# Kernel tuning notes

Measured on AMD Instinct MI355X. Metric: run time of the kernel, lower is better.

The kernel has to match this reference:

```python
import jax, jax.numpy as jnp
import numpy as np

HID = 128
MAX_NODES = 100000
MAX_EDGES = 300000
EVT_LEN = 4096
NUM_NODE = 20000
NUM_EDGE = 320000
# EVENT_TYPE_ID_MAP: pad=0 start=1 end=2 node-add=3 node-delete=4 edge-add=5 edge-delete=6
NODE_ADD, NODE_DEL = 3, 4


def time_encode(t, time_w, time_b):
    # TimeEncoder: cos(Linear(1 -> hidden)(t))
    return jnp.cos(t[..., None] * time_w + time_b)


def gru_cell(x, h, w_ih, w_hh, b_ih, b_hh):
    gi = x @ w_ih.T + b_ih
    gh = h @ w_hh.T + b_hh
    i_r, i_z, i_n = jnp.split(gi, 3, axis=-1)
    h_r, h_z, h_n = jnp.split(gh, 3, axis=-1)
    r = jax.nn.sigmoid(i_r + h_r)
    z = jax.nn.sigmoid(i_z + h_z)
    n = jnp.tanh(i_n + r * h_n)
    return (1.0 - z) * n + z * h


def setup_inputs() -> dict:
    key = jax.random.key(0)
    ks = jax.random.split(key, 32)
    H = HID
    s = 0.05
    inp = {}
    inp["event_type_ids"] = jax.random.randint(ks[0], (EVT_LEN,), 0, 7)
    inp["src_ids"] = jax.random.randint(ks[1], (EVT_LEN,), 0, MAX_NODES)
    inp["src_mask"] = (jax.random.uniform(ks[2], (EVT_LEN,)) > 0.3).astype(jnp.float32)
    inp["dst_ids"] = jax.random.randint(ks[3], (EVT_LEN,), 0, MAX_NODES)
    inp["dst_mask"] = (jax.random.uniform(ks[4], (EVT_LEN,)) > 0.3).astype(jnp.float32)
    inp["event_edge_ids"] = jax.random.randint(ks[5], (EVT_LEN,), 0, MAX_EDGES)
    inp["event_embeddings"] = jax.random.normal(ks[6], (EVT_LEN, H), dtype=jnp.float32)
    inp["event_mask"] = (jax.random.uniform(ks[7], (EVT_LEN,)) > 0.2).astype(jnp.float32)
    inp["event_timestamps"] = jax.random.uniform(ks[8], (EVT_LEN,)) * 100.0
    inp["node_ids"] = jax.random.randint(ks[9], (NUM_NODE,), 0, MAX_NODES)
    inp["edge_ids"] = jax.random.randint(ks[10], (NUM_EDGE,), 0, MAX_EDGES)
    inp["edge_index"] = jax.random.randint(ks[11], (2, NUM_EDGE), 0, NUM_NODE)
    inp["time"] = 100
    # persistent-buffer state
    inp["memory"] = jax.random.normal(ks[12], (MAX_NODES, H), dtype=jnp.float32) * s
    inp["last_update"] = jax.random.uniform(ks[13], (MAX_EDGES,)) * 50.0
    inp["node_features"] = jax.random.normal(ks[14], (MAX_NODES, H), dtype=jnp.float32) * s
    inp["edge_features"] = jax.random.normal(ks[15], (MAX_EDGES, H), dtype=jnp.float32) * s
    # TimeEncoder params (Linear(1, H))
    inp["time_w"] = jax.random.normal(ks[16], (H,), dtype=jnp.float32) * s
    inp["time_b"] = jax.random.normal(ks[17], (H,), dtype=jnp.float32) * s
    # GRUCell(5H -> H)
    inp["gru_w_ih"] = jax.random.normal(ks[18], (3 * H, 5 * H), dtype=jnp.float32) * s
    inp["gru_w_hh"] = jax.random.normal(ks[19], (3 * H, H), dtype=jnp.float32) * s
    inp["gru_b_ih"] = jax.random.normal(ks[20], (3 * H,), dtype=jnp.float32) * s
    inp["gru_b_hh"] = jax.random.normal(ks[21], (3 * H,), dtype=jnp.float32) * s
    # TransformerConv(H, H, heads=1, edge_dim=2H)
    inp["wq"] = jax.random.normal(ks[22], (H, H), dtype=jnp.float32) * s
    inp["bq"] = jax.random.normal(ks[23], (H,), dtype=jnp.float32) * s
    inp["wk"] = jax.random.normal(ks[24], (H, H), dtype=jnp.float32) * s
    inp["bk"] = jax.random.normal(ks[25], (H,), dtype=jnp.float32) * s
    inp["wv"] = jax.random.normal(ks[26], (H, H), dtype=jnp.float32) * s
    inp["bv"] = jax.random.normal(ks[27], (H,), dtype=jnp.float32) * s
    inp["we"] = jax.random.normal(ks[28], (H, 2 * H), dtype=jnp.float32) * s  # lin_edge, no bias
    inp["wskip"] = jax.random.normal(ks[29], (H, H), dtype=jnp.float32) * s
    inp["bskip"] = jax.random.normal(ks[30], (H,), dtype=jnp.float32) * s
    return inp


def reference(event_type_ids, src_ids, src_mask, dst_ids, dst_mask, event_edge_ids,
              event_embeddings, event_mask, event_timestamps, node_ids, edge_ids,
              edge_index, time, memory, last_update, node_features, edge_features,
              time_w, time_b, gru_w_ih, gru_w_hh, gru_b_ih, gru_b_hh,
              wq, bq, wk, bk, wv, bv, we, wskip, bskip):
    H = HID
    # ---- message() ----
    L = event_type_ids.shape[0]
    type_embs = jnp.broadcast_to(event_type_ids[:, None].astype(memory.dtype), (L, H))
    src_embs = memory[src_ids] * src_mask[:, None]
    dst_embs = memory[dst_ids] * dst_mask[:, None]
    edge_last = last_update[event_edge_ids]
    rel_ts = event_timestamps - edge_last * dst_mask
    is_node_ev = ((event_type_ids == NODE_ADD) | (event_type_ids == NODE_DEL)).astype(event_timestamps.dtype)
    ts_emb = time_encode(event_timestamps * is_node_ev + rel_ts * dst_mask, time_w, time_b) * event_mask[:, None]
    src_msgs = jnp.concatenate([type_embs, src_embs, dst_embs, ts_emb, event_embeddings], axis=1) * event_mask[:, None]
    dst_msgs = jnp.concatenate([type_embs, dst_embs, src_embs, ts_emb, event_embeddings], axis=1) * dst_mask[:, None]
    # ---- agg_message(): scatter-mean over node ids ----
    def agg(msgs, ids):
        s = jax.ops.segment_sum(msgs, ids, num_segments=MAX_NODES)
        c = jax.ops.segment_sum(jnp.ones((msgs.shape[0],), msgs.dtype), ids, num_segments=MAX_NODES)
        return s / jnp.maximum(c, 1.0)[:, None]
    agg_src = agg(src_msgs, src_ids)
    agg_dst = agg(dst_msgs, dst_ids)
    # ---- GRU memory update on unique ids ----
    # torch: memory[cat(uniq_src, uniq_dst)] = rnn(...); reads use pre-update memory,
    # dst writes come after src writes so they override on overlap. Duplicate ids in
    # src_ids carry identical per-id values, so scatter-set is equivalent to unique().
    new_src = gru_cell(agg_src[src_ids], memory[src_ids], gru_w_ih, gru_w_hh, gru_b_ih, gru_b_hh)
    new_dst = gru_cell(agg_dst[dst_ids], memory[dst_ids], gru_w_ih, gru_w_hh, gru_b_ih, gru_b_hh)
    memory = memory.at[src_ids].set(new_src)
    memory = memory.at[dst_ids].set(new_dst)
    # ---- edge attributes ----
    rel_t = time - last_update[edge_ids]
    rel_t_embs = time_encode(rel_t, time_w, time_b)
    edge_attr = jnp.concatenate([rel_t_embs, edge_features[edge_ids]], axis=-1)  # (E, 2H)
    # ---- TransformerConv (heads=1, concat, root_weight) ----
    x = node_features[node_ids] + memory[node_ids]  # (N, H)
    src, dst = edge_index[0], edge_index[1]
    q = x @ wq.T + bq
    k = x @ wk.T + bk
    v = x @ wv.T + bv
    e = edge_attr @ we.T  # lin_edge (no bias)
    alpha = jnp.sum(q[dst] * (k[src] + e), axis=-1) / jnp.sqrt(jnp.asarray(H, x.dtype))
    amax = jax.ops.segment_max(alpha, dst, num_segments=x.shape[0])
    ex = jnp.exp(alpha - amax[dst])
    denom = jax.ops.segment_sum(ex, dst, num_segments=x.shape[0])
    p = ex / jnp.maximum(denom[dst], 1e-16)
    out = jax.ops.segment_sum(p[:, None] * (v[src] + e), dst, num_segments=x.shape[0])
    return out + x @ wskip.T + bskip
```

## Files before the change

kernel.cpp:

```cpp
#include <hip/hip_runtime.h>
#include <math.h>

#define HID   128
#define MAXN  100000
#define MAXE  300000
#define EVT   4096
#define NNODE 20000
#define NEDGE 320000

typedef unsigned short u16;
typedef __attribute__((ext_vector_type(8))) short bf16x8;
typedef __attribute__((ext_vector_type(4))) float f32x4;

#define OFF_WIHB      0u
#define OFF_WHHB      491520u
#define OFF_WEB       589824u
#define OFF_WALLB     655360u
#define OFF_BALL      851968u
#define BASE2         855040u
#define OFF_HEAD_SRC  (BASE2 + 0u)
#define OFF_HEAD_DST  (BASE2 + 400128u)
#define OFF_CNT_SRC   (BASE2 + 800256u)
#define OFF_CNT_DST   (BASE2 + 1200384u)
#define OFF_CHAIN_SRC (BASE2 + 1600512u)
#define OFF_CHAIN_DST (BASE2 + 1616896u)
#define OFF_XGB       (BASE2 + 22572032u)
#define OFF_HG        (BASE2 + 33057792u)
#define OFF_HGB       (BASE2 + 37252096u)
#define OFF_GI        (BASE2 + 39349248u)
#define OFF_GH        (BASE2 + 51932160u)
#define OFF_XB        (BASE2 + 1703936u)
#define OFF_QKVSE     (BASE2 + 7000064u)
#undef OFF_XB
#undef OFF_QKVSE
#define OFF_XB        (BASE2 + 1703936u)
#define OFF_QKVSE     (BASE2 + 6823936u)
#define OFF_KVB       (BASE2 + 68263936u)
#define OFF_DEG       (BASE2 + 78503936u)
#define OFF_OFFS      (BASE2 + 78584064u)
#define OFF_CURSOR    (BASE2 + 78664192u)
#define OFF_SORTED    (BASE2 + 78744320u)
#define OFF_SACCB     (BASE2 + 80024320u)

__device__ __forceinline__ float sigmoidf_(float x) { return 1.f / (1.f + __expf(-x)); }
__device__ __forceinline__ u16 f2b(float f) {
    unsigned u = __float_as_uint(f);
    unsigned r = (u + 0x7fffu + ((u >> 16) & 1u)) >> 16;
    return (u16)r;
}
__device__ __forceinline__ float b2f(unsigned h) { return __uint_as_float(h << 16); }

__global__ void k_prep(const float* __restrict__ w_ih, const float* __restrict__ w_hh,
                       const float* __restrict__ we,
                       const float* __restrict__ wq, const float* __restrict__ wk_,
                       const float* __restrict__ wv, const float* __restrict__ wskip,
                       const float* __restrict__ bq, const float* __restrict__ bk,
                       const float* __restrict__ bv, const float* __restrict__ bskip,
                       u16* __restrict__ w_ih_b, u16* __restrict__ w_hh_b,
                       u16* __restrict__ we_b, u16* __restrict__ Wallb,
                       float* __restrict__ ball, int* __restrict__ deg,
                       char* __restrict__ zbase) {
    int b = blockIdx.x, t = threadIdx.x;
    if (b < 960) {
        int i = b * 256 + t;
        w_ih_b[i] = f2b(w_ih[i]);
        return;
    }
    b -= 960;
    if (b < 192) {
        int i = b * 256 + t;
        w_hh_b[i] = f2b(w_hh[i]);
        return;
    }
    b -= 192;
    if (b < 128) {
        int i = b * 256 + t;
        we_b[i] = f2b(we[i]);
        return;
    }
    b -= 128;
    if (b < 79) {
        int i = b * 256 + t;
        if (i < NNODE) deg[i] = 0;
        return;
    }
    b -= 79;
    if (b < 384) {
        int idx = b * 256 + t;
        int row = idx >> 7;
        int k = idx & 127;
        float v;
        if (row < 128)      v = wq[row * 128 + k];
        else if (row < 256) v = wk_[(row - 128) * 128 + k];
        else if (row < 384) v = wv[(row - 256) * 128 + k];
        else if (row < 512) v = wskip[(row - 384) * 128 + k];
        else {
            int j = row - 512;
            float a = 0.f;
            for (int t2 = 0; t2 < 128; t2++) a += wq[t2 * 128 + k] * we[t2 * 256 + j];
            v = a;
        }
        Wallb[row * 128 + k] = f2b(v);
        if (k == 0) {
            float bb;
            if (row < 128)      bb = bq[row];
            else if (row < 256) bb = bk[row - 128];
            else if (row < 384) bb = bv[row - 256];
            else if (row < 512) bb = bskip[row - 384];
            else { int j = row - 512; float a = 0.f; for (int t2 = 0; t2 < 128; t2++) a += bq[t2] * we[t2 * 256 + j]; bb = a; }
            ball[row] = bb;
        }
        return;
    }
    b -= 384;
    const int NFF = 50016;
    uint4 ff = make_uint4(0xFFFFFFFFu, 0xFFFFFFFFu, 0xFFFFFFFFu, 0xFFFFFFFFu);
    uint4 zz = make_uint4(0u, 0u, 0u, 0u);
    int idx = b * 256 + t;
    int stride = 257 * 256;
    uint4* pff = (uint4*)zbase;
    uint4* pzz = (uint4*)(zbase + 800256);
    for (int i = idx; i < NFF; i += stride) pff[i] = ff;
    for (int i = idx; i < NFF; i += stride) pzz[i] = zz;
}

__global__ void k_msg_tables(const int* __restrict__ et_ids, const int* __restrict__ src_ids,
                          const float* __restrict__ src_mask, const int* __restrict__ dst_ids,
                          const float* __restrict__ dst_mask, const int* __restrict__ ev_eids,
                          const float* __restrict__ ev_emb, const float* __restrict__ ev_mask,
                          const float* __restrict__ ev_ts, const float* __restrict__ memory,
                          const float* __restrict__ last_update, const float* __restrict__ time_w,
                          const float* __restrict__ time_b,
                          int* __restrict__ head_src, int* __restrict__ head_dst,
                          int* __restrict__ cnt_src, int* __restrict__ cnt_dst,
                          int* __restrict__ chain_src, int* __restrict__ chain_dst,
                          const int* __restrict__ eidx, int* __restrict__ deg,
                          u16* __restrict__ Xgb, float* __restrict__ Hg, u16* __restrict__ Hgb) {
    int b = blockIdx.x, t = threadIdx.x;
    if (b >= EVT) {
        int bb = b - EVT;
        if (bb < 32) {
            int i = bb * 128 + t;
            int s = src_ids[i], d = dst_ids[i];
            chain_src[i] = atomicExch(&head_src[s], i);
            atomicAdd(&cnt_src[s], 1);
            chain_dst[i] = atomicExch(&head_dst[d], i);
            atomicAdd(&cnt_dst[d], 1);
        } else {
            int j = (bb - 32) * 128 + t;
            atomicAdd(&deg[eidx[NEDGE + j]], 1);
        }
        return;
    }
    int i = b;
    int c = t;
    int et = et_ids[i];
    float sm = src_mask[i], dm = dst_mask[i], em = ev_mask[i], ts = ev_ts[i];
    int sid = src_ids[i], did = dst_ids[i], eid = ev_eids[i];
    float isnode = (et == 3 || et == 4) ? 1.f : 0.f;
    float rel = ts - last_update[eid] * dm;
    float tval = ts * isnode + rel * dm;
    float tse = __cosf(tval * time_w[c] + time_b[c]) * em;
    float typ = (float)et;
    float sv_raw = memory[(size_t)sid * HID + c];
    float dv_raw = memory[(size_t)did * HID + c];
    float sv = sv_raw * sm;
    float dv = dv_raw * dm;
    float ev = ev_emb[(size_t)i * HID + c];
    Hg[(size_t)i * HID + c] = sv_raw;
    Hgb[(size_t)i * HID + c] = f2b(sv_raw);
    Hg[(size_t)(EVT + i) * HID + c] = dv_raw;
    Hgb[(size_t)(EVT + i) * HID + c] = f2b(dv_raw);
    u16* xs = Xgb + (size_t)i * 640;
    xs[c] = f2b(typ * em); xs[128 + c] = f2b(sv * em); xs[256 + c] = f2b(dv * em);
    xs[384 + c] = f2b(tse * em); xs[512 + c] = f2b(ev * em);
    u16* xd = Xgb + (size_t)(EVT + i) * 640;
    xd[c] = f2b(typ * dm); xd[128 + c] = f2b(dv * dm); xd[256 + c] = f2b(sv * dm);
    xd[384 + c] = f2b(tse * dm); xd[512 + c] = f2b(ev * dm);
}

__global__ void k_fix(const int* __restrict__ src_ids, const int* __restrict__ dst_ids,
                      const int* __restrict__ head_src, const int* __restrict__ head_dst,
                      const int* __restrict__ chain_src, const int* __restrict__ chain_dst,
                      const int* __restrict__ cnt_src, const int* __restrict__ cnt_dst,
                      const int* __restrict__ et_ids, const float* __restrict__ src_mask,
                      const float* __restrict__ dst_mask, const int* __restrict__ ev_eids,
                      const float* __restrict__ ev_emb, const float* __restrict__ ev_mask,
                      const float* __restrict__ ev_ts, const float* __restrict__ memory,
                      const float* __restrict__ last_update, const float* __restrict__ time_w,
                      const float* __restrict__ time_b, u16* __restrict__ Xgb) {
    int r = blockIdx.x, c = threadIdx.x;
    bool is_src = (r < EVT);
    int id = is_src ? src_ids[r] : dst_ids[r - EVT];
    int cnt = is_src ? cnt_src[id] : cnt_dst[id];
    if (cnt < 2) return;
    float own = memory[(size_t)id * HID + c];
    float tw = time_w[c], tb = time_b[c];
    float a0 = 0.f, a1 = 0.f, a2 = 0.f, a3 = 0.f, a4 = 0.f;
    int j = is_src ? head_src[id] : head_dst[id];
    for (int k = 0; k < cnt; ++k) {
        int et = et_ids[j];
        float sm = src_mask[j], dm = dst_mask[j], em = ev_mask[j], ts = ev_ts[j];
        int eid = ev_eids[j];
        float isnode = (et == 3 || et == 4) ? 1.f : 0.f;
        float rel = ts - last_update[eid] * dm;
        float tval = ts * isnode + rel * dm;
        float tse = __cosf(tval * tw + tb);
        float ev = ev_emb[(size_t)j * HID + c];
        float typ = (float)et;
        if (is_src) {
            float sv = own * sm;
            float dv = memory[(size_t)dst_ids[j] * HID + c] * dm;
            float tsm = tse * em;
            a0 += typ * em; a1 += sv * em; a2 += dv * em;
            a3 += tsm * em; a4 += ev * em;
            j = chain_src[j];
        } else {
            float dv = own * dm;
            float sv = memory[(size_t)src_ids[j] * HID + c] * sm;
            float tsm = tse * em;
            a0 += typ * dm; a1 += dv * dm; a2 += sv * dm;
            a3 += tsm * dm; a4 += ev * dm;
            j = chain_dst[j];
        }
    }
    float inv = 1.f / (float)cnt;
    u16* x = Xgb + (size_t)r * 640;
    x[c] = f2b(a0 * inv); x[128 + c] = f2b(a1 * inv); x[256 + c] = f2b(a2 * inv);
    x[384 + c] = f2b(a3 * inv); x[512 + c] = f2b(a4 * inv);
}

__device__ __forceinline__ void gemm_tile(const u16* __restrict__ A, const u16* __restrict__ W,
                                          const float* __restrict__ bias, float* __restrict__ C,
                                          u16* __restrict__ KVb, int M, int N, int K, int acc,
                                          u16* Als, u16* Wls) {
    int tid = threadIdx.x;
    int bm = blockIdx.x * 128, bn = blockIdx.y * 128;
    int wave = tid >> 6, lane = tid & 63;
    int wm = (wave & 1) * 64, wn = (wave >> 1) * 64;
    int l15 = lane & 15, quad = lane >> 4;
    f32x4 accf[4][4] = {};
    for (int k0 = 0; k0 < K; k0 += 32) {
#pragma unroll
        for (int h = 0; h < 2; ++h) {
            int ch = tid + h * 256;
            int row = ch >> 2, kc = (ch & 3) * 8;
            int gr = bm + row;
            float4 av = make_float4(0.f, 0.f, 0.f, 0.f);
            if (gr < M) av = *(const float4*)(A + (size_t)gr * K + k0 + kc);
            *(float4*)&Als[row * 40 + kc] = av;
            int wr = bn + row;
            float4 wv_ = *(const float4*)(W + (size_t)wr * K + k0 + kc);
            *(float4*)&Wls[row * 40 + kc] = wv_;
        }
        __syncthreads();
        bf16x8 af[4], bfr[4];
#pragma unroll
        for (int r = 0; r < 4; ++r)
            af[r] = *(const bf16x8*)&Als[(wm + r * 16 + l15) * 40 + quad * 8];
#pragma unroll
        for (int c2 = 0; c2 < 4; ++c2)
            bfr[c2] = *(const bf16x8*)&Wls[(wn + c2 * 16 + l15) * 40 + quad * 8];
#pragma unroll
        for (int r = 0; r < 4; ++r)
#pragma unroll
            for (int c2 = 0; c2 < 4; ++c2)
                accf[r][c2] = __builtin_amdgcn_mfma_f32_16x16x32_bf16(af[r], bfr[c2], accf[r][c2], 0, 0, 0);
        __syncthreads();
    }
#pragma unroll
    for (int r = 0; r < 4; ++r) {
#pragma unroll
        for (int c2 = 0; c2 < 4; ++c2) {
            int ncol = bn + wn + c2 * 16 + l15;
            float bv = bias ? bias[ncol] : 0.f;
#pragma unroll
            for (int reg = 0; reg < 4; ++reg) {
                int mrow = bm + wm + r * 16 + quad * 4 + reg;
                if (mrow >= M) continue;
                float v = accf[r][c2][reg] + bv;
                if (KVb && ncol >= 128 && ncol < 384) {
                    KVb[(size_t)mrow * 256 + (ncol - 128)] = f2b(v);
                } else {
                    if (acc) v += C[(size_t)mrow * N + ncol];
                    C[(size_t)mrow * N + ncol] = v;
                }
            }
        }
    }
}

__global__ __launch_bounds__(256) void k_gemm_mfma(const u16* __restrict__ A,
                                                   const u16* __restrict__ W,
                                                   const float* __restrict__ bias,
                                                   float* __restrict__ C,
                                                   u16* __restrict__ KVb,
                                                   int M, int N, int K, int acc) {
    __shared__ u16 Als[128 * 40];
    __shared__ u16 Wls[128 * 40];
    gemm_tile(A, W, bias, C, KVb, M, N, K, acc, Als, Wls);
}

__global__ __launch_bounds__(256) void k_gemm_qkvse(const u16* __restrict__ A,
                                                    const u16* __restrict__ W,
                                                    const float* __restrict__ bias,
                                                    float* __restrict__ C,
                                                    u16* __restrict__ KVb,
                                                    const int* __restrict__ eidx,
                                                    int* __restrict__ cursor,
                                                    int* __restrict__ sorted) {
    __shared__ u16 Als[128 * 40];
    __shared__ u16 Wls[128 * 40];
    if (blockIdx.y == 6) {
        int j = blockIdx.x * 256 + threadIdx.x;
        for (; j < NEDGE; j += 157 * 256) {
            int d = eidx[NEDGE + j];
            int pos = atomicAdd(&cursor[d], 1);
            sorted[pos] = j;
        }
        return;
    }
    gemm_tile(A, W, bias, C, KVb, NNODE, 768, 128, 0, Als, Wls);
}

__global__ __launch_bounds__(256) void k_gemm_dual(const u16* __restrict__ A0, const u16* __restrict__ W0,
                                                   const float* __restrict__ b0, float* __restrict__ C0,
                                                   const u16* __restrict__ A1, const u16* __restrict__ W1,
                                                   const float* __restrict__ b1, float* __restrict__ C1) {
    __shared__ u16 Als[128 * 40];
    __shared__ u16 Wls[128 * 40];
    if (blockIdx.z == 0) gemm_tile(A0, W0, b0, C0, nullptr, 2 * EVT, 384, 640, 0, Als, Wls);
    else                 gemm_tile(A1, W1, b1, C1, nullptr, 2 * EVT, 384, 128, 0, Als, Wls);
}

__global__ void k_gru_scatter(const float* __restrict__ Gi, const float* __restrict__ Gh,
                              const float* __restrict__ Hg, const int* __restrict__ src_ids,
                              const int* __restrict__ dst_ids, const int* __restrict__ cnt_dst,
                              float* __restrict__ memory) {
    int r = blockIdx.x, c = threadIdx.x;
    const float* gi = Gi + (size_t)r * 384;
    const float* gh = Gh + (size_t)r * 384;
    float rg = sigmoidf_(gi[c] + gh[c]);
    float z  = sigmoidf_(gi[128 + c] + gh[128 + c]);
    float n  = tanhf(gi[256 + c] + rg * gh[256 + c]);
    float h0 = Hg[(size_t)r * HID + c];
    float h  = (1.f - z) * n + z * h0;
    if (r < EVT) {
        int sid = src_ids[r];
        if (cnt_dst[sid] == 0) memory[(size_t)sid * HID + c] = h;
    } else {
        int did = dst_ids[r - EVT];
        memory[(size_t)did * HID + c] = h;
    }
}

__global__ __launch_bounds__(1024) void k_x_scan(const int* __restrict__ node_ids,
                                                 const float* __restrict__ nf,
                                                 const float* __restrict__ memory,
                                                 u16* __restrict__ Xb,
                                                 const int* __restrict__ deg,
                                                 int* __restrict__ offs,
                                                 int* __restrict__ cursor) {
    __shared__ int wsum[16];
    int p = blockIdx.x, t = threadIdx.x;
    if (p < 2500) {
        int row = p * 8 + (t >> 7), c = t & 127;
        int nid = node_ids[row];
        Xb[(size_t)row * HID + c] = f2b(nf[(size_t)nid * HID + c] + memory[(size_t)nid * HID + c]);
        return;
    }
    int lane = t & 63, w = t >> 6;
    int carry = 0;
    const int N4 = NNODE / 4;
    for (int base = 0; base < N4; base += 1024) {
        int i4 = base + t;
        int4 v = make_int4(0, 0, 0, 0);
        if (i4 < N4) v = ((const int4*)deg)[i4];
        int s = v.x + v.y + v.z + v.w;
        int x = s;
#pragma unroll
        for (int d = 1; d < 64; d <<= 1) { int y = __shfl_up(x, d, 64); if (lane >= d) x += y; }
        if (lane == 63) wsum[w] = x;
        __syncthreads();
        int add = 0, tot = 0;
        for (int k2 = 0; k2 < 16; ++k2) { int ss = wsum[k2]; if (k2 < w) add += ss; tot += ss; }
        if (i4 < N4) {
            int e = carry + add + x - s;
            int4 o;
            o.x = e;
            o.y = e + v.x;
            o.z = o.y + v.y;
            o.w = o.z + v.z;
            ((int4*)offs)[i4] = o;
            ((int4*)cursor)[i4] = o;
        }
        carry += tot;
        __syncthreads();
    }
    if (t == 0) offs[NNODE] = NEDGE;
}

__global__ __launch_bounds__(256) void k_node(const float* __restrict__ QK,
        const u16* __restrict__ KVb, const int* __restrict__ offs,
        const int* __restrict__ sorted, const int* __restrict__ eidx,
        const int* __restrict__ edge_ids, const float* __restrict__ last_update,
        const float* __restrict__ time_w, const float* __restrict__ time_b,
        const float* __restrict__ ef, const int* __restrict__ tptr,
        float* __restrict__ out, u16* __restrict__ saccb) {
    int wave = threadIdx.x >> 6, lane = threadIdx.x & 63;
    int n = blockIdx.x * 4 + wave;
    int c = 2 * lane;
    const float* base = QK + (size_t)n * 768;
    float2 qd   = *(const float2*)(base + c);
    float2 skip = *(const float2*)(base + 384 + c);
    float2 qet  = *(const float2*)(base + 512 + c);
    float2 qef  = *(const float2*)(base + 640 + c);
    float2 tw   = *(const float2*)(time_w + c);
    float2 tb   = *(const float2*)(time_b + c);
    float tf = (float)(*tptr);
    int start = offs[n], end = offs[n + 1];
    int deg = end - start;
    if (deg == 0) {
        *(float2*)(out + (size_t)n * HID + c) = skip;
        *(unsigned*)(saccb + (size_t)n * 256 + c) = 0u;
        *(unsigned*)(saccb + (size_t)n * 256 + 128 + c) = 0u;
        return;
    }
    float m = -1e30f, l_ = 0.f;
    float va0 = 0.f, va1 = 0.f, s00 = 0.f, s01 = 0.f, s10 = 0.f, s11 = 0.f;
    for (int cb = start; cb < end; cb += 64) {
        int cnt = end - cb; if (cnt > 64) cnt = 64;
        int s_l = 0, eid_l = 0; float rt_l = 0.f;
        if (lane < cnt) {
            int j = sorted[cb + lane];
            s_l = eidx[j];
            eid_l = edge_ids[j];
            rt_l = tf - last_update[eid_l];
        }
        for (int e0 = 0; e0 < cnt; e0 += 4) {
            float pv[4], cv0[4], cv1[4], vx[4], vy[4], ex[4], ey[4];
#pragma unroll
            for (int i = 0; i < 4; ++i) {
                int idx = e0 + i;
                int sel = (idx < cnt) ? idx : e0;
                int s   = __shfl(s_l, sel, 64);
                int eid = __shfl(eid_l, sel, 64);
                float rt = __shfl(rt_l, sel, 64);
                unsigned kvp = *(const unsigned*)(KVb + (size_t)s * 256 + c);
                unsigned vvp = *(const unsigned*)(KVb + (size_t)s * 256 + 128 + c);
                float2 ev = *(const float2*)(ef + (size_t)eid * HID + c);
                float k0f = b2f(kvp & 0xffffu), k1f = b2f(kvp >> 16);
                vx[i] = b2f(vvp & 0xffffu); vy[i] = b2f(vvp >> 16);
                cv0[i] = __cosf(rt * tw.x + tb.x);
                cv1[i] = __cosf(rt * tw.y + tb.y);
                ex[i] = ev.x; ey[i] = ev.y;
                pv[i] = qd.x * k0f + qd.y * k1f + qet.x * cv0[i] + qet.y * cv1[i]
                      + qef.x * ev.x + qef.y * ev.y;
            }
#pragma unroll
            for (int msk = 32; msk > 0; msk >>= 1) {
#pragma unroll
                for (int i = 0; i < 4; ++i) pv[i] += __shfl_xor(pv[i], msk, 64);
            }
            float al[4];
#pragma unroll
            for (int i = 0; i < 4; ++i)
                al[i] = (e0 + i < cnt) ? pv[i] * 0.08838834764831845f : -1e30f;
            float gm = fmaxf(fmaxf(al[0], al[1]), fmaxf(al[2], al[3]));
            if (gm > m) {
                float fac = __expf(m - gm);
                l_ *= fac; va0 *= fac; va1 *= fac;
                s00 *= fac; s01 *= fac; s10 *= fac; s11 *= fac;
                m = gm;
            }
#pragma unroll
            for (int i = 0; i < 4; ++i) {
                float w = __expf(al[i] - m);
                l_ += w;
                va0 += w * vx[i]; va1 += w * vy[i];
                s00 += w * cv0[i]; s01 += w * cv1[i];
                s10 += w * ex[i]; s11 += w * ey[i];
            }
        }
    }
    float inv = 1.f / fmaxf(l_, 1e-16f);
    float2 o; o.x = va0 * inv + skip.x; o.y = va1 * inv + skip.y;
    *(float2*)(out + (size_t)n * HID + c) = o;
    unsigned p0 = (unsigned)f2b(s00 * inv) | ((unsigned)f2b(s01 * inv) << 16);
    unsigned p1 = (unsigned)f2b(s10 * inv) | ((unsigned)f2b(s11 * inv) << 16);
    *(unsigned*)(saccb + (size_t)n * 256 + c) = p0;
    *(unsigned*)(saccb + (size_t)n * 256 + 128 + c) = p1;
}

extern "C" void kernel_launch(void* const* d_in, const int* in_sizes, int n_in,
                              void* d_out, int out_size, void* d_ws, size_t ws_size,
                              hipStream_t stream) {
    const int*   et_ids        = (const int*)d_in[0];
    const int*   src_ids       = (const int*)d_in[1];
    const float* src_mask      = (const float*)d_in[2];
    const int*   dst_ids       = (const int*)d_in[3];
    const float* dst_mask      = (const float*)d_in[4];
    const int*   ev_eids       = (const int*)d_in[5];
    const float* ev_emb        = (const float*)d_in[6];
    const float* ev_mask       = (const float*)d_in[7];
    const float* ev_ts         = (const float*)d_in[8];
    const int*   node_ids      = (const int*)d_in[9];
    const int*   edge_ids      = (const int*)d_in[10];
    const int*   edge_index    = (const int*)d_in[11];
    const int*   tptr          = (const int*)d_in[12];
    float*       memory        = (float*)d_in[13];
    const float* last_update   = (const float*)d_in[14];
    const float* node_features = (const float*)d_in[15];
    const float* edge_features = (const float*)d_in[16];
    const float* time_w        = (const float*)d_in[17];
    const float* time_b        = (const float*)d_in[18];
    const float* w_ih          = (const float*)d_in[19];
    const float* w_hh          = (const float*)d_in[20];
    const float* b_ih          = (const float*)d_in[21];
    const float* b_hh          = (const float*)d_in[22];
    const float* wq            = (const float*)d_in[23];
    const float* bq            = (const float*)d_in[24];
    const float* wk            = (const float*)d_in[25];
    const float* bk            = (const float*)d_in[26];
    const float* wv            = (const float*)d_in[27];
    const float* bv            = (const float*)d_in[28];
    const float* we            = (const float*)d_in[29];
    const float* wskip         = (const float*)d_in[30];
    const float* bskip         = (const float*)d_in[31];
    float* out = (float*)d_out;
    char*  wsb = (char*)d_ws;

    u16*   w_ih_b   = (u16*)(wsb + OFF_WIHB);
    u16*   w_hh_b   = (u16*)(wsb + OFF_WHHB);
    u16*   we_b     = (u16*)(wsb + OFF_WEB);
    u16*   Wallb    = (u16*)(wsb + OFF_WALLB);
    float* ball     = (float*)(wsb + OFF_BALL);
    int*   head_src = (int*)(wsb + OFF_HEAD_SRC);
    int*   head_dst = (int*)(wsb + OFF_HEAD_DST);
    int*   cnt_src  = (int*)(wsb + OFF_CNT_SRC);
    int*   cnt_dst  = (int*)(wsb + OFF_CNT_DST);
    int*   chain_src= (int*)(wsb + OFF_CHAIN_SRC);
    int*   chain_dst= (int*)(wsb + OFF_CHAIN_DST);
    u16*   Xgb      = (u16*)(wsb + OFF_XGB);
    float* Hg       = (float*)(wsb + OFF_HG);
    u16*   Hgb      = (u16*)(wsb + OFF_HGB);
    float* Gi       = (float*)(wsb + OFF_GI);
    float* Gh       = (float*)(wsb + OFF_GH);
    u16*   Xb       = (u16*)(wsb + OFF_XB);
    float* QKVSE    = (float*)(wsb + OFF_QKVSE);
    u16*   KVb      = (u16*)(wsb + OFF_KVB);
    int*   deg      = (int*)(wsb + OFF_DEG);
    int*   offs     = (int*)(wsb + OFF_OFFS);
    int*   cursor   = (int*)(wsb + OFF_CURSOR);
    int*   sorted   = (int*)(wsb + OFF_SORTED);
    u16*   saccb    = (u16*)(wsb + OFF_SACCB);

    k_prep<<<2000, 256, 0, stream>>>(w_ih, w_hh, we, wq, wk, wv, wskip, bq, bk, bv, bskip,
                                     w_ih_b, w_hh_b, we_b, Wallb, ball, deg, wsb + OFF_HEAD_SRC);
    k_msg_tables<<<6628, 128, 0, stream>>>(et_ids, src_ids, src_mask, dst_ids, dst_mask, ev_eids,
                                           ev_emb, ev_mask, ev_ts, memory, last_update, time_w, time_b,
                                           head_src, head_dst, cnt_src, cnt_dst, chain_src, chain_dst,
                                           edge_index, deg, Xgb, Hg, Hgb);
    k_fix<<<2 * EVT, 128, 0, stream>>>(src_ids, dst_ids, head_src, head_dst, chain_src, chain_dst,
                                       cnt_src, cnt_dst, et_ids, src_mask, dst_mask, ev_eids,
                                       ev_emb, ev_mask, ev_ts, memory, last_update, time_w, time_b,
                                       Xgb);
    k_gemm_dual<<<dim3(64, 3, 2), 256, 0, stream>>>(Xgb, w_ih_b, b_ih, Gi,
                                                    Hgb, w_hh_b, b_hh, Gh);
    k_gru_scatter<<<2 * EVT, 128, 0, stream>>>(Gi, Gh, Hg, src_ids, dst_ids, cnt_dst, memory);
    k_x_scan<<<2501, 1024, 0, stream>>>(node_ids, node_features, memory, Xb, deg, offs, cursor);
    k_gemm_qkvse<<<dim3(157, 7), 256, 0, stream>>>(Xb, Wallb, ball, QKVSE, KVb,
                                                   edge_index, cursor, sorted);
    k_node<<<NNODE / 4, 256, 0, stream>>>(QKVSE, KVb, offs, sorted, edge_index, edge_ids,
                                          last_update, time_w, time_b, edge_features, tptr,
                                          out, saccb);
    k_gemm_mfma<<<dim3(157, 1), 256, 0, stream>>>(saccb, we_b, nullptr, out, nullptr, NNODE, 128, 256, 1);
}
```

Measured before the change: 490.1 us.

## Fuse GRU GEMMs and gate epilogue into one kernel; store QKV projections as bf16

Concatenates the input and hidden GRU weights and inputs into one [X|H] bf16 layout. A single k_gates kernel computes the r, z and n gate accumulators with MFMA and applies the GRU update and memory scatter in its epilogue, which removes the Gi/Gh fp32 intermediates and the separate gru_scatter kernel. The QKV projection GEMM now writes all outputs as bf16 and keeps only the skip columns in fp32, so the gather traffic in k_node shrinks. The cost is that k_gates launches only 64 blocks, each doing several serial K passes, so that stage has low occupancy, and storing q in bf16 adds rounding error.

Measured after the change: 538.1 us. 1.1x slower.

```diff
diff --git a/kernel.cpp b/kernel.cpp
--- a/kernel.cpp
+++ b/kernel.cpp
@@ -12,8 +12,7 @@
 typedef __attribute__((ext_vector_type(8))) short bf16x8;
 typedef __attribute__((ext_vector_type(4))) float f32x4;
 
-#define OFF_WIHB      0u
-#define OFF_WHHB      491520u
+#define OFF_WCATB     0u
 #define OFF_WEB       589824u
 #define OFF_WALLB     655360u
 #define OFF_BALL      851968u
@@ -24,23 +23,16 @@
 #define OFF_CNT_DST   (BASE2 + 1200384u)
 #define OFF_CHAIN_SRC (BASE2 + 1600512u)
 #define OFF_CHAIN_DST (BASE2 + 1616896u)
-#define OFF_XGB       (BASE2 + 22572032u)
-#define OFF_HG        (BASE2 + 33057792u)
-#define OFF_HGB       (BASE2 + 37252096u)
-#define OFF_GI        (BASE2 + 39349248u)
-#define OFF_GH        (BASE2 + 51932160u)
-#define OFF_XB        (BASE2 + 1703936u)
-#define OFF_QKVSE     (BASE2 + 7000064u)
-#undef OFF_XB
-#undef OFF_QKVSE
-#define OFF_XB        (BASE2 + 1703936u)
-#define OFF_QKVSE     (BASE2 + 6823936u)
-#define OFF_KVB       (BASE2 + 68263936u)
-#define OFF_DEG       (BASE2 + 78503936u)
-#define OFF_OFFS      (BASE2 + 78584064u)
-#define OFF_CURSOR    (BASE2 + 78664192u)
-#define OFF_SORTED    (BASE2 + 78744320u)
-#define OFF_SACCB     (BASE2 + 80024320u)
+#define OFF_XHB       (BASE2 + 1703936u)
+#define OFF_HG        (BASE2 + 14286848u)
+#define OFF_XB        (BASE2 + 20000000u)
+#define OFF_QB        (BASE2 + 25120000u)
+#define OFF_SKIPF     (BASE2 + 55840000u)
+#define OFF_DEG       (BASE2 + 66080000u)
+#define OFF_OFFS      (BASE2 + 66160128u)
+#define OFF_CURSOR    (BASE2 + 66240256u)
+#define OFF_SORTED    (BASE2 + 66320384u)
+#define OFF_SACCB     (BASE2 + 67600384u)
 
 __device__ __forceinline__ float sigmoidf_(float x) { return 1.f / (1.f + __expf(-x)); }
 __device__ __forceinline__ u16 f2b(float f) {
@@ -56,23 +48,18 @@
                        const float* __restrict__ wv, const float* __restrict__ wskip,
                        const float* __restrict__ bq, const float* __restrict__ bk,
                        const float* __restrict__ bv, const float* __restrict__ bskip,
-                       u16* __restrict__ w_ih_b, u16* __restrict__ w_hh_b,
-                       u16* __restrict__ we_b, u16* __restrict__ Wallb,
-                       float* __restrict__ ball, int* __restrict__ deg,
-                       char* __restrict__ zbase) {
+                       u16* __restrict__ Wcatb, u16* __restrict__ we_b,
+                       u16* __restrict__ Wallb, float* __restrict__ ball,
+                       int* __restrict__ deg, char* __restrict__ zbase) {
     int b = blockIdx.x, t = threadIdx.x;
-    if (b < 960) {
-        int i = b * 256 + t;
-        w_ih_b[i] = f2b(w_ih[i]);
-        return;
-    }
-    b -= 960;
-    if (b < 192) {
-        int i = b * 256 + t;
-        w_hh_b[i] = f2b(w_hh[i]);
-        return;
-    }
-    b -= 192;
+    if (b < 1152) {
+        int idx = b * 256 + t;
+        int row = idx / 768, col = idx % 768;
+        float v = (col < 640) ? w_ih[row * 640 + col] : w_hh[row * 128 + (col - 640)];
+        Wcatb[idx] = f2b(v);
+        return;
+    }
+    b -= 1152;
     if (b < 128) {
         int i = b * 256 + t;
         we_b[i] = f2b(we[i]);
@@ -135,7 +122,7 @@
                           int* __restrict__ cnt_src, int* __restrict__ cnt_dst,
                           int* __restrict__ chain_src, int* __restrict__ chain_dst,
                           const int* __restrict__ eidx, int* __restrict__ deg,
-                          u16* __restrict__ Xgb, float* __restrict__ Hg, u16* __restrict__ Hgb) {
+                          u16* __restrict__ XHb, float* __restrict__ Hg) {
     int b = blockIdx.x, t = threadIdx.x;
     if (b >= EVT) {
         int bb = b - EVT;
@@ -168,15 +155,15 @@
     float dv = dv_raw * dm;
     float ev = ev_emb[(size_t)i * HID + c];
     Hg[(size_t)i * HID + c] = sv_raw;
-    Hgb[(size_t)i * HID + c] = f2b(sv_raw);
     Hg[(size_t)(EVT + i) * HID + c] = dv_raw;
-    Hgb[(size_t)(EVT + i) * HID + c] = f2b(dv_raw);
-    u16* xs = Xgb + (size_t)i * 640;
+    u16* xs = XHb + (size_t)i * 768;
     xs[c] = f2b(typ * em); xs[128 + c] = f2b(sv * em); xs[256 + c] = f2b(dv * em);
     xs[384 + c] = f2b(tse * em); xs[512 + c] = f2b(ev * em);
-    u16* xd = Xgb + (size_t)(EVT + i) * 640;
+    xs[640 + c] = f2b(sv_raw);
+    u16* xd = XHb + (size_t)(EVT + i) * 768;
     xd[c] = f2b(typ * dm); xd[128 + c] = f2b(dv * dm); xd[256 + c] = f2b(sv * dm);
     xd[384 + c] = f2b(tse * dm); xd[512 + c] = f2b(ev * dm);
+    xd[640 + c] = f2b(dv_raw);
 }
 
 __global__ void k_fix(const int* __restrict__ src_ids, const int* __restrict__ dst_ids,
@@ -188,7 +175,7 @@
                       const float* __restrict__ ev_emb, const float* __restrict__ ev_mask,
                       const float* __restrict__ ev_ts, const float* __restrict__ memory,
                       const float* __restrict__ last_update, const float* __restrict__ time_w,
-                      const float* __restrict__ time_b, u16* __restrict__ Xgb) {
+                      const float* __restrict__ time_b, u16* __restrict__ XHb) {
     int r = blockIdx.x, c = threadIdx.x;
     bool is_src = (r < EVT);
     int id = is_src ? src_ids[r] : dst_ids[r - EVT];
@@ -225,14 +212,104 @@
         }
     }
     float inv = 1.f / (float)cnt;
-    u16* x = Xgb + (size_t)r * 640;
+    u16* x = XHb + (size_t)r * 768;
     x[c] = f2b(a0 * inv); x[128 + c] = f2b(a1 * inv); x[256 + c] = f2b(a2 * inv);
     x[384 + c] = f2b(a3 * inv); x[512 + c] = f2b(a4 * inv);
 }
 
+__device__ __forceinline__ void gate_pass(const u16* __restrict__ A, int lda,
+                                          const u16* __restrict__ W, int ldw, int K,
+                                          f32x4 acc[4][4], u16* Als, u16* Wls,
+                                          int bm, int wm, int wn, int l15, int quad, int tid) {
+    for (int k0 = 0; k0 < K; k0 += 32) {
+#pragma unroll
+        for (int h = 0; h < 2; ++h) {
+            int ch = tid + h * 256;
+            int row = ch >> 2, kc = (ch & 3) * 8;
+            *(float4*)&Als[row * 40 + kc] = *(const float4*)(A + (size_t)(bm + row) * lda + k0 + kc);
+            *(float4*)&Wls[row * 40 + kc] = *(const float4*)(W + (size_t)row * ldw + k0 + kc);
+        }
+        __syncthreads();
+        bf16x8 af[4], bfr[4];
+#pragma unroll
+        for (int r = 0; r < 4; ++r)
+            af[r] = *(const bf16x8*)&Als[(wm + r * 16 + l15) * 40 + quad * 8];
+#pragma unroll
+        for (int c2 = 0; c2 < 4; ++c2)
+            bfr[c2] = *(const bf16x8*)&Wls[(wn + c2 * 16 + l15) * 40 + quad * 8];
+#pragma unroll
+        for (int r = 0; r < 4; ++r)
+#pragma unroll
+            for (int c2 = 0; c2 < 4; ++c2)
+                acc[r][c2] = __builtin_amdgcn_mfma_f32_16x16x32_bf16(af[r], bfr[c2], acc[r][c2], 0, 0, 0);
+        __syncthreads();
+    }
+}
+
+__global__ __launch_bounds__(256, 1) void k_gates(const u16* __restrict__ XHb,
+        const u16* __restrict__ Wcat, const float* __restrict__ b_ih,
+        const float* __restrict__ b_hh, const float* __restrict__ Hg,
+        const int* __restrict__ src_ids, const int* __restrict__ dst_ids,
+        const int* __restrict__ cnt_dst, float* __restrict__ memory) {
+    __shared__ u16 Als[128 * 40];
+    __shared__ u16 Wls[128 * 40];
+    int tid = threadIdx.x;
+    int bm = blockIdx.x * 128;
+    int wave = tid >> 6, lane = tid & 63;
+    int wm = (wave & 1) * 64, wn = (wave >> 1) * 64;
+    int l15 = lane & 15, quad = lane >> 4;
+    f32x4 acc_h[4][4] = {};
+    f32x4 acc_a[4][4] = {};
+    f32x4 acc_i[4][4] = {};
+    gate_pass(XHb + 640, 768, Wcat + (size_t)256 * 768 + 640, 768, 128,
+              acc_h, Als, Wls, bm, wm, wn, l15, quad, tid);
+    gate_pass(XHb, 768, Wcat, 768, 768, acc_a, Als, Wls, bm, wm, wn, l15, quad, tid);
+#pragma unroll
+    for (int r = 0; r < 4; ++r)
+#pragma unroll
+        for (int c2 = 0; c2 < 4; ++c2) {
+            int ncol = wn + c2 * 16 + l15;
+            float bs0 = b_ih[ncol] + b_hh[ncol];
+            float bh2 = b_hh[256 + ncol];
+#pragma unroll
+            for (int reg = 0; reg < 4; ++reg) {
+                float rg = sigmoidf_(acc_a[r][c2][reg] + bs0);
+                acc_h[r][c2][reg] = rg * (acc_h[r][c2][reg] + bh2);
+                acc_a[r][c2][reg] = 0.f;
+            }
+        }
+    gate_pass(XHb, 768, Wcat + (size_t)128 * 768, 768, 768,
+              acc_a, Als, Wls, bm, wm, wn, l15, quad, tid);
+    gate_pass(XHb, 768, Wcat + (size_t)256 * 768, 768, 640,
+              acc_i, Als, Wls, bm, wm, wn, l15, quad, tid);
+#pragma unroll
+    for (int r = 0; r < 4; ++r)
+#pragma unroll
+        for (int c2 = 0; c2 < 4; ++c2) {
+            int ncol = wn + c2 * 16 + l15;
+            float bz = b_ih[128 + ncol] + b_hh[128 + ncol];
+            float bi2 = b_ih[256 + ncol];
+#pragma unroll
+            for (int reg = 0; reg < 4; ++reg) {
+                int mrow = bm + wm + r * 16 + quad * 4 + reg;
+                float z = sigmoidf_(acc_a[r][c2][reg] + bz);
+                float n = tanhf(acc_i[r][c2][reg] + bi2 + acc_h[r][c2][reg]);
+                float h0 = Hg[(size_t)mrow * HID + ncol];
+                float h = (1.f - z) * n + z * h0;
+                if (mrow < EVT) {
+                    int sid = src_ids[mrow];
+                    if (cnt_dst[sid] == 0) memory[(size_t)sid * HID + ncol] = h;
+                } else {
+                    int did = dst_ids[mrow - EVT];
+                    memory[(size_t)did * HID + ncol] = h;
+                }
+            }
+        }
+}
+
 __device__ __forceinline__ void gemm_tile(const u16* __restrict__ A, const u16* __restrict__ W,
                                           const float* __restrict__ bias, float* __restrict__ C,
-                                          u16* __restrict__ KVb, int M, int N, int K, int acc,
+                                          int M, int N, int K, int acc,
                                           u16* Als, u16* Wls) {
     int tid = threadIdx.x;
     int bm = blockIdx.x * 128, bn = blockIdx.y * 128;
@@ -279,12 +356,8 @@
                 int mrow = bm + wm + r * 16 + quad * 4 + reg;
                 if (mrow >= M) continue;
                 float v = accf[r][c2][reg] + bv;
-                if (KVb && ncol >= 128 && ncol < 384) {
-                    KVb[(size_t)mrow * 256 + (ncol - 128)] = f2b(v);
-                } else {
-                    if (acc) v += C[(size_t)mrow * N + ncol];
-                    C[(size_t)mrow * N + ncol] = v;
-                }
+                if (acc) v += C[(size_t)mrow * N + ncol];
+                C[(size_t)mrow * N + ncol] = v;
             }
         }
     }
@@ -294,18 +367,17 @@
                                                    const u16* __restrict__ W,
                                                    const float* __restrict__ bias,
                                                    float* __restrict__ C,
-                                                   u16* __restrict__ KVb,
                                                    int M, int N, int K, int acc) {
     __shared__ u16 Als[128 * 40];
     __shared__ u16 Wls[128 * 40];
-    gemm_tile(A, W, bias, C, KVb, M, N, K, acc, Als, Wls);
+    gemm_tile(A, W, bias, C, M, N, K, acc, Als, Wls);
 }
 
 __global__ __launch_bounds__(256) void k_gemm_qkvse(const u16* __restrict__ A,
                                                     const u16* __restrict__ W,
                                                     const float* __restrict__ bias,
-                                                    float* __restrict__ C,
-                                                    u16* __restrict__ KVb,
+                                                    u16* __restrict__ QB,
+                                                    float* __restrict__ SkipF,
                                                     const int* __restrict__ eidx,
                                                     int* __restrict__ cursor,
                                                     int* __restrict__ sorted) {
@@ -320,37 +392,56 @@
         }
         return;
     }
-    gemm_tile(A, W, bias, C, KVb, NNODE, 768, 128, 0, Als, Wls);
-}
-
-__global__ __launch_bounds__(256) void k_gemm_dual(const u16* __restrict__ A0, const u16* __restrict__ W0,
-                                                   const float* __restrict__ b0, float* __restrict__ C0,
-                                                   const u16* __restrict__ A1, const u16* __restrict__ W1,
-                                                   const float* __restrict__ b1, float* __restrict__ C1) {
-    __shared__ u16 Als[128 * 40];
-    __shared__ u16 Wls[128 * 40];
-    if (blockIdx.z == 0) gemm_tile(A0, W0, b0, C0, nullptr, 2 * EVT, 384, 640, 0, Als, Wls);
-    else                 gemm_tile(A1, W1, b1, C1, nullptr, 2 * EVT, 384, 128, 0, Als, Wls);
-}
-
-__global__ void k_gru_scatter(const float* __restrict__ Gi, const float* __restrict__ Gh,
-                              const float* __restrict__ Hg, const int* __restrict__ src_ids,
-                              const int* __restrict__ dst_ids, const int* __restrict__ cnt_dst,
-                              float* __restrict__ memory) {
-    int r = blockIdx.x, c = threadIdx.x;
-    const float* gi = Gi + (size_t)r * 384;
-    const float* gh = Gh + (size_t)r * 384;
-    float rg = sigmoidf_(gi[c] + gh[c]);
-    float z  = sigmoidf_(gi[128 + c] + gh[128 + c]);
-    float n  = tanhf(gi[256 + c] + rg * gh[256 + c]);
-    float h0 = Hg[(size_t)r * HID + c];
-    float h  = (1.f - z) * n + z * h0;
-    if (r < EVT) {
-        int sid = src_ids[r];
-        if (cnt_dst[sid] == 0) memory[(size_t)sid * HID + c] = h;
-    } else {
-        int did = dst_ids[r - EVT];
-        memory[(size_t)did * HID + c] = h;
+    int tid = threadIdx.x;
+    int bm = blockIdx.x * 128, bn = blockIdx.y * 128;
+    int wave = tid >> 6, lane = tid & 63;
+    int wm = (wave & 1) * 64, wn = (wave >> 1) * 64;
+    int l15 = lane & 15, quad = lane >> 4;
+    f32x4 accf[4][4] = {};
+    for (int k0 = 0; k0 < 128; k0 += 32) {
+#pragma unroll
+        for (int h = 0; h < 2; ++h) {
+            int ch = tid + h * 256;
+            int row = ch >> 2, kc = (ch & 3) * 8;
+            int gr = bm + row;
+            float4 av = make_float4(0.f, 0.f, 0.f, 0.f);
+            if (gr < NNODE) av = *(const float4*)(A + (size_t)gr * 128 + k0 + kc);
+            *(float4*)&Als[row * 40 + kc] = av;
+            int wr = bn + row;
+            float4 wv_ = *(const float4*)(W + (size_t)wr * 128 + k0 + kc);
+            *(float4*)&Wls[row * 40 + kc] = wv_;
+        }
+        __syncthreads();
+        bf16x8 af[4], bfr[4];
+#pragma unroll
+        for (int r = 0; r < 4; ++r)
+            af[r] = *(const bf16x8*)&Als[(wm + r * 16 + l15) * 40 + quad * 8];
+#pragma unroll
+        for (int c2 = 0; c2 < 4; ++c2)
+            bfr[c2] = *(const bf16x8*)&Wls[(wn + c2 * 16 + l15) * 40 + quad * 8];
+#pragma unroll
+        for (int r = 0; r < 4; ++r)
+#pragma unroll
+            for (int c2 = 0; c2 < 4; ++c2)
+                accf[r][c2] = __builtin_amdgcn_mfma_f32_16x16x32_bf16(af[r], bfr[c2], accf[r][c2], 0, 0, 0);
+        __syncthreads();
+    }
+#pragma unroll
+    for (int r = 0; r < 4; ++r) {
+#pragma unroll
+        for (int c2 = 0; c2 < 4; ++c2) {
+            int ncol = bn + wn + c2 * 16 + l15;
+            float bv = bias[ncol];
+#pragma unroll
+            for (int reg = 0; reg < 4; ++reg) {
+                int mrow = bm + wm + r * 16 + quad * 4 + reg;
+                if (mrow >= NNODE) continue;
+                float v = accf[r][c2][reg] + bv;
+                QB[(size_t)mrow * 768 + ncol] = f2b(v);
+                if (ncol >= 384 && ncol < 512)
+                    SkipF[(size_t)mrow * 128 + (ncol - 384)] = v;
+            }
+        }
     }
 }
 
@@ -400,8 +491,8 @@
     if (t == 0) offs[NNODE] = NEDGE;
 }
 
-__global__ __launch_bounds__(256) void k_node(const float* __restrict__ QK,
-        const u16* __restrict__ KVb, const int* __restrict__ offs,
+__global__ __launch_bounds__(256) void k_node(const u16* __restrict__ QB,
+        const float* __restrict__ SkipF, const int* __restrict__ offs,
         const int* __restrict__ sorted, const int* __restrict__ eidx,
         const int* __restrict__ edge_ids, const float* __restrict__ last_update,
         const float* __restrict__ time_w, const float* __restrict__ time_b,
@@ -410,11 +501,15 @@
     int wave = threadIdx.x >> 6, lane = threadIdx.x & 63;
     int n = blockIdx.x * 4 + wave;
     int c = 2 * lane;
-    const float* base = QK + (size_t)n * 768;
-    float2 qd   = *(const float2*)(base + c);
-    float2 skip = *(const float2*)(base + 384 + c);
-    float2 qet  = *(const float2*)(base + 512 + c);
-    float2 qef  = *(const float2*)(base + 640 + c);
+    const u16* rowq = QB + (size_t)n * 768;
+    unsigned qw  = *(const unsigned*)(rowq + c);
+    unsigned qtw = *(const unsigned*)(rowq + 512 + c);
+    unsigned qfw = *(const unsigned*)(rowq + 640 + c);
+    float2 qd, qet, qef;
+    qd.x  = b2f(qw & 0xffffu);  qd.y  = b2f(qw >> 16);
+    qet.x = b2f(qtw & 0xffffu); qet.y = b2f(qtw >> 16);
+    qef.x = b2f(qfw & 0xffffu); qef.y = b2f(qfw >> 16);
+    float2 skip = *(const float2*)(SkipF + (size_t)n * HID + c);
     float2 tw   = *(const float2*)(time_w + c);
     float2 tb   = *(const float2*)(time_b + c);
     float tf = (float)(*tptr);
@@ -446,8 +541,8 @@
                 int s   = __shfl(s_l, sel, 64);
                 int eid = __shfl(eid_l, sel, 64);
                 float rt = __shfl(rt_l, sel, 64);
-                unsigned kvp = *(const unsigned*)(KVb + (size_t)s * 256 + c);
-                unsigned vvp = *(const unsigned*)(KVb + (size_t)s * 256 + 128 + c);
+                unsigned kvp = *(const unsigned*)(QB + (size_t)s * 768 + 128 + c);
+                unsigned vvp = *(const unsigned*)(QB + (size_t)s * 768 + 256 + c);
                 float2 ev = *(const float2*)(ef + (size_t)eid * HID + c);
                 float k0f = b2f(kvp & 0xffffu), k1f = b2f(kvp >> 16);
                 vx[i] = b2f(vvp & 0xffffu); vy[i] = b2f(vvp >> 16);
@@ -530,8 +625,7 @@
     float* out = (float*)d_out;
     char*  wsb = (char*)d_ws;
 
-    u16*   w_ih_b   = (u16*)(wsb + OFF_WIHB);
-    u16*   w_hh_b   = (u16*)(wsb + OFF_WHHB);
+    u16*   Wcatb    = (u16*)(wsb + OFF_WCATB);
     u16*   we_b     = (u16*)(wsb + OFF_WEB);
     u16*   Wallb    = (u16*)(wsb + OFF_WALLB);
     float* ball     = (float*)(wsb + OFF_BALL);
@@ -541,14 +635,11 @@
     int*   cnt_dst  = (int*)(wsb + OFF_CNT_DST);
     int*   chain_src= (int*)(wsb + OFF_CHAIN_SRC);
     int*   chain_dst= (int*)(wsb + OFF_CHAIN_DST);
-    u16*   Xgb      = (u16*)(wsb + OFF_XGB);
+    u16*   XHb      = (u16*)(wsb + OFF_XHB);
     float* Hg       = (float*)(wsb + OFF_HG);
-    u16*   Hgb      = (u16*)(wsb + OFF_HGB);
-    float* Gi       = (float*)(wsb + OFF_GI);
-    float* Gh       = (float*)(wsb + OFF_GH);
     u16*   Xb       = (u16*)(wsb + OFF_XB);
-    float* QKVSE    = (float*)(wsb + OFF_QKVSE);
-    u16*   KVb      = (u16*)(wsb + OFF_KVB);
+    u16*   QB       = (u16*)(wsb + OFF_QB);
+    float* SkipF    = (float*)(wsb + OFF_SKIPF);
     int*   deg      = (int*)(wsb + OFF_DEG);
     int*   offs     = (int*)(wsb + OFF_OFFS);
     int*   cursor   = (int*)(wsb + OFF_CURSOR);
@@ -556,23 +647,21 @@
     u16*   saccb    = (u16*)(wsb + OFF_SACCB);
 
     k_prep<<<2000, 256, 0, stream>>>(w_ih, w_hh, we, wq, wk, wv, wskip, bq, bk, bv, bskip,
-                                     w_ih_b, w_hh_b, we_b, Wallb, ball, deg, wsb + OFF_HEAD_SRC);
+                                     Wcatb, we_b, Wallb, ball, deg, wsb + OFF_HEAD_SRC);
     k_msg_tables<<<6628, 128, 0, stream>>>(et_ids, src_ids, src_mask, dst_ids, dst_mask, ev_eids,
                                            ev_emb, ev_mask, ev_ts, memory, last_update, time_w, time_b,
                                            head_src, head_dst, cnt_src, cnt_dst, chain_src, chain_dst,
-                                           edge_index, deg, Xgb, Hg, Hgb);
+                                           edge_index, deg, XHb, Hg);
     k_fix<<<2 * EVT, 128, 0, stream>>>(src_ids, dst_ids, head_src, head_dst, chain_src, chain_dst,
                                        cnt_src, cnt_dst, et_ids, src_mask, dst_mask, ev_eids,
                                        ev_emb, ev_mask, ev_ts, memory, last_update, time_w, time_b,
-                                       Xgb);
-    k_gemm_dual<<<dim3(64, 3, 2), 256, 0, stream>>>(Xgb, w_ih_b, b_ih, Gi,
-                                                    Hgb, w_hh_b, b_hh, Gh);
-    k_gru_scatter<<<2 * EVT, 128, 0, stream>>>(Gi, Gh, Hg, src_ids, dst_ids, cnt_dst, memory);
+                                       XHb);
+    k_gates<<<64, 256, 0, stream>>>(XHb, Wcatb, b_ih, b_hh, Hg, src_ids, dst_ids, cnt_dst, memory);
     k_x_scan<<<2501, 1024, 0, stream>>>(node_ids, node_features, memory, Xb, deg, offs, cursor);
-    k_gemm_qkvse<<<dim3(157, 7), 256, 0, stream>>>(Xb, Wallb, ball, QKVSE, KVb,
+    k_gemm_qkvse<<<dim3(157, 7), 256, 0, stream>>>(Xb, Wallb, ball, QB, SkipF,
                                                    edge_index, cursor, sorted);
-    k_node<<<NNODE / 4, 256, 0, stream>>>(QKVSE, KVb, offs, sorted, edge_index, edge_ids,
+    k_node<<<NNODE / 4, 256, 0, stream>>>(QB, SkipF, offs, sorted, edge_index, edge_ids,
                                           last_update, time_w, time_b, edge_features, tptr,
                                           out, saccb);
-    k_gemm_mfma<<<dim3(157, 1), 256, 0, stream>>>(saccb, we_b, nullptr, out, nullptr, NNODE, 128, 256, 1);
-}
+    k_gemm_mfma<<<dim3(157, 1), 256, 0, stream>>>(saccb, we_b, nullptr, out, NNODE, 128, 256, 1);
+}
```
